# Performance work log

Measured on AMD Instinct MI355X. Metric: run time of the kernel, lower is better.

## Reference

```python
import jax, jax.numpy as jnp
import numpy as np

B, N = 32, 1024


def _pose(points, rot, trans):
    # points: [B,N,3], rot: [B,3,3], trans: [B,3]
    # torch.bmm(points, rot.transpose(1,2)) + trans.unsqueeze(1)
    return jnp.einsum('bni,bji->bnj', points, rot) + trans[:, None, :]


def _l2_dis(pred, target):
    # [B,N] pointwise L2 distance
    return jnp.linalg.norm(pred - target, axis=2)


def _cd_dis(pred, target):
    # symmetric Chamfer-style distance, [B,N]
    p2 = jnp.sum(pred * pred, axis=2)          # [B,N]
    t2 = jnp.sum(target * target, axis=2)      # [B,N]
    cross = jnp.einsum('bnd,bmd->bnm', pred, target)  # [B,N,N]
    d2 = jnp.maximum(p2[:, :, None] + t2[:, None, :] - 2.0 * cross, 0.0)
    dis = jnp.sqrt(d2)                          # [B,N,N]
    dis1 = jnp.min(dis, axis=2)                 # min over target -> [B,N]
    dis2 = jnp.min(dis, axis=1)                 # min over pred   -> [B,N]
    return 0.5 * (dis1 + dis2)


def setup_inputs() -> dict:
    key = jax.random.key(0)
    ks = jax.random.split(key, 8)
    return {
        'delta_rot_pred': jax.random.normal(ks[0], (B, 3, 3), jnp.float32),
        'delta_trans_pred': jax.random.normal(ks[1], (B, 3), jnp.float32),
        'trans_cur': jax.random.normal(ks[2], (B, 3), jnp.float32),
        'rot_cur': jax.random.normal(ks[3], (B, 3, 3), jnp.float32),
        'rot_gt': jax.random.normal(ks[4], (B, 3, 3), jnp.float32),
        'trans_gt': jax.random.normal(ks[5], (B, 3), jnp.float32),
        'points_tmp': jax.random.normal(ks[6], (B, N, 3), jnp.float32),
        'sym_flag': jax.random.uniform(ks[7], (B,), jnp.float32),
    }


def reference(delta_rot_pred, delta_trans_pred, trans_cur, rot_cur, rot_gt, trans_gt, points_tmp, sym_flag):
    posed_pred = _pose(points_tmp, delta_rot_pred, delta_trans_pred)   # [B,N,3]
    posed_gt = _pose(points_tmp, rot_gt, trans_gt)                     # [B,N,3]
    posed_refined = _pose(posed_pred, rot_cur, trans_cur)              # [B,N,3]
    l2 = _l2_dis(posed_refined, posed_gt)                              # [B,N]
    cd = _cd_dis(posed_refined, posed_gt)                              # [B,N]
    per_point = (1.0 - sym_flag)[:, None] * l2 + sym_flag[:, None] * cd
    loss_pose = per_point.mean(axis=1).mean()
    return loss_pose
```

## Files before the change

kernel.cpp:

```cpp
#include <hip/hip_runtime.h>
#include <math.h>

constexpr int B = 32;
constexpr int N = 1024;
constexpr int OCTS = 16;
constexpr int NBLK = B * OCTS;
constexpr int NTHR = 512;
constexpr unsigned short ONE_BF = 0x3F80;

typedef __attribute__((ext_vector_type(8))) short short8;
typedef __attribute__((ext_vector_type(4))) float f32x4;

__device__ __forceinline__ void split_bf(float x, unsigned short& h, unsigned short& l) {
    union { float f; unsigned u; } a; a.f = x;
    unsigned r = (a.u + 0x7FFFu + ((a.u >> 16) & 1u)) >> 16;
    h = (unsigned short)r;
    union { unsigned u; float f; } hb; hb.u = r << 16;
    union { float f; unsigned u; } d; d.f = x - hb.f;
    l = (unsigned short)((d.u + 0x7FFFu + ((d.u >> 16) & 1u)) >> 16);
}
__device__ __forceinline__ unsigned short neg2bf(unsigned short h) {
    return (unsigned short)((h & 0x7FFFu) ? (unsigned short)((h ^ 0x8000u) + 0x0080u)
                                          : (unsigned short)0);
}
__device__ __forceinline__ unsigned pk(unsigned short a, unsigned short b) {
    return (unsigned)a | ((unsigned)b << 16);
}

__global__ __launch_bounds__(NTHR, 4) void chamfer_mfma(
    const float* __restrict__ dR,
    const float* __restrict__ dt,
    const float* __restrict__ tc,
    const float* __restrict__ Rc,
    const float* __restrict__ G,
    const float* __restrict__ g,
    const float* __restrict__ pts,
    const float* __restrict__ sym,
    float* __restrict__ partial)
{
    __shared__ __align__(16) unsigned short Bp[N][16];
    __shared__ __align__(16) unsigned short Bg[N][16];
    __shared__ __align__(16) unsigned short Ap[64][32];
    __shared__ __align__(16) unsigned short Ag[64][32];
    __shared__ float wsum[8];

    const int blk = blockIdx.x;
    const int b   = blk >> 4;
    const int oct = blk & 15;
    const int t   = threadIdx.x;

    const float* dRb = dR + b * 9;
    const float* Rcb = Rc + b * 9;
    const float* Gb  = G  + b * 9;
    const float* dtb = dt + b * 3;
    const float* tcb = tc + b * 3;
    const float* gb  = g  + b * 3;
    const float symb = sym[b];

    float M[9], v[3];
    #pragma unroll
    for (int j = 0; j < 3; ++j) {
        #pragma unroll
        for (int i = 0; i < 3; ++i)
            M[j*3+i] = Rcb[j*3+0]*dRb[0*3+i] + Rcb[j*3+1]*dRb[1*3+i] + Rcb[j*3+2]*dRb[2*3+i];
        v[j] = Rcb[j*3+0]*dtb[0] + Rcb[j*3+1]*dtb[1] + Rcb[j*3+2]*dtb[2] + tcb[j];
    }

    float acc = 0.f;

    {
        const float2* P2 = (const float2*)(pts + (size_t)b * N * 3);
        const float2 u0 = P2[3*t + 0];
        const float2 u1 = P2[3*t + 1];
        const float2 u2 = P2[3*t + 2];
        const float pxs[2] = {u0.x, u1.y};
        const float pys[2] = {u0.y, u2.x};
        const float pzs[2] = {u1.x, u2.y};
        #pragma unroll
        for (int s = 0; s < 2; ++s) {
            const int i = 2*t + s;
            const float px = pxs[s], py = pys[s], pz = pzs[s];
            const float ax = fmaf(M[0],px, fmaf(M[1],py, fmaf(M[2],pz, v[0])));
            const float ay = fmaf(M[3],px, fmaf(M[4],py, fmaf(M[5],pz, v[1])));
            const float az = fmaf(M[6],px, fmaf(M[7],py, fmaf(M[8],pz, v[2])));
            const float cx = fmaf(Gb[0],px, fmaf(Gb[1],py, fmaf(Gb[2],pz, gb[0])));
            const float cy = fmaf(Gb[3],px, fmaf(Gb[4],py, fmaf(Gb[5],pz, gb[1])));
            const float cz = fmaf(Gb[6],px, fmaf(Gb[7],py, fmaf(Gb[8],pz, gb[2])));
            const float a2 = ax*ax + ay*ay + az*az;
            const float c2 = cx*cx + cy*cy + cz*cz;

            if (oct == 0) {
                const float dx = ax - cx, dy = ay - cy, dz = az - cz;
                acc += (1.f - symb) * sqrtf(dx*dx + dy*dy + dz*dz);
            }

            unsigned short axh,axl, ayh,ayl, azh,azl, anh,anl;
            unsigned short cxh,cxl, cyh,cyl, czh,czl, cnh,cnl;
            split_bf(ax,axh,axl); split_bf(ay,ayh,ayl); split_bf(az,azh,azl); split_bf(a2,anh,anl);
            split_bf(cx,cxh,cxl); split_bf(cy,cyh,cyl); split_bf(cz,czh,czl); split_bf(c2,cnh,cnl);

            uint4 bp0 = {pk(axh,ayh), pk(azh,axh), pk(ayh,azh), pk(axl,ayl)};
            uint4 bp1 = {pk(azl,axl), pk(ayl,azl), pk(ONE_BF,ONE_BF), pk(anh,anl)};
            *(uint4*)&Bp[i][0] = bp0; *(uint4*)&Bp[i][8] = bp1;
            uint4 bg0 = {pk(cxh,cyh), pk(czh,cxh), pk(cyh,czh), pk(cxl,cyl)};
            uint4 bg1 = {pk(czl,cxl), pk(cyl,czl), pk(ONE_BF,ONE_BF), pk(cnh,cnl)};
            *(uint4*)&Bg[i][0] = bg0; *(uint4*)&Bg[i][8] = bg1;

            if ((i >> 6) == oct) {
                const int lr = i & 63;
                const unsigned short nxh=neg2bf(axh), nyh=neg2bf(ayh), nzh=neg2bf(azh);
                const unsigned short nxl=neg2bf(axl), nyl=neg2bf(ayl), nzl=neg2bf(azl);
                uint4 a0 = {pk(nxh,nyh), pk(nzh,nxl), pk(nyl,nzl), pk(nxh,nyh)};
                uint4 a1 = {pk(nzh,nxl), pk(nyl,nzl), pk(anh,anl), pk(ONE_BF,ONE_BF)};
                uint4 zz = {0,0,0,0};
                *(uint4*)&Ap[lr][0] = a0; *(uint4*)&Ap[lr][8]  = a1;
                *(uint4*)&Ap[lr][16] = zz; *(uint4*)&Ap[lr][24] = zz;
                const unsigned short mxh=neg2bf(cxh), myh=neg2bf(cyh), mzh=neg2bf(czh);
                const unsigned short mxl=neg2bf(cxl), myl=neg2bf(cyl), mzl=neg2bf(czl);
                uint4 c0 = {pk(mxh,myh), pk(mzh,mxl), pk(myl,mzl), pk(mxh,myh)};
                uint4 c1 = {pk(mzh,mxl), pk(myl,mzl), pk(cnh,cnl), pk(ONE_BF,ONE_BF)};
                *(uint4*)&Ag[lr][0] = c0; *(uint4*)&Ag[lr][8]  = c1;
                *(uint4*)&Ag[lr][16] = zz; *(uint4*)&Ag[lr][24] = zz;
            }
        }
    }
    __syncthreads();

    const int w    = t >> 6;
    const int lane = t & 63;
    const int side = w >> 2;
    const int strip= w & 3;
    const int col  = lane & 15;
    const int kg   = lane >> 4;

    const unsigned short* Abase = (side ? &Ag[0][0] : &Ap[0][0])
                                  + (strip*16 + col) * 32 + kg * 8;
    const unsigned short* Bbase = (side ? &Bp[0][0] : &Bg[0][0])
                                  + col * 16 + (kg & 1) * 8;

    const short8 av = *(const short8*)Abase;
    const f32x4 zero = {0.f, 0.f, 0.f, 0.f};
    float r0 = 3.4e38f, r1 = 3.4e38f, r2 = 3.4e38f, r3 = 3.4e38f;

    #pragma unroll 8
    for (int tile = 0; tile < 64; ++tile) {
        const short8 bv = *(const short8*)(Bbase + tile * 256);
        const f32x4 c = __builtin_amdgcn_mfma_f32_16x16x32_bf16(av, bv, zero, 0, 0, 0);
        r0 = fminf(r0, c[0]); r1 = fminf(r1, c[1]);
        r2 = fminf(r2, c[2]); r3 = fminf(r3, c[3]);
    }

    #pragma unroll
    for (int m = 1; m <= 8; m <<= 1) {
        r0 = fminf(r0, __shfl_xor(r0, m));
        r1 = fminf(r1, __shfl_xor(r1, m));
        r2 = fminf(r2, __shfl_xor(r2, m));
        r3 = fminf(r3, __shfl_xor(r3, m));
    }
    if (col == 0) {
        acc += 0.5f * symb * (sqrtf(fmaxf(r0, 0.f)) + sqrtf(fmaxf(r1, 0.f)) +
                              sqrtf(fmaxf(r2, 0.f)) + sqrtf(fmaxf(r3, 0.f)));
    }

    #pragma unroll
    for (int m = 1; m <= 32; m <<= 1) acc += __shfl_xor(acc, m);
    if (lane == 0) wsum[w] = acc;
    __syncthreads();
    if (t == 0) {
        float s = 0.f;
        #pragma unroll
        for (int j = 0; j < 8; ++j) s += wsum[j];
        partial[blk] = s;
    }
}

__global__ __launch_bounds__(128) void chamfer_final(
    const float* __restrict__ partial, float* __restrict__ out)
{
    __shared__ float wsum[2];
    const int t = threadIdx.x;
    const float4 v = ((const float4*)partial)[t];
    float a = (v.x + v.y) + (v.z + v.w);
    #pragma unroll
    for (int m = 1; m <= 32; m <<= 1) a += __shfl_xor(a, m);
    if ((t & 63) == 0) wsum[t >> 6] = a;
    __syncthreads();
    if (t == 0) out[0] = (wsum[0] + wsum[1]) * (1.0f / (float)(B * N));
}

extern "C" void kernel_launch(void* const* d_in, const int* in_sizes, int n_in,
                              void* d_out, int out_size, void* d_ws, size_t ws_size,
                              hipStream_t stream) {
    const float* dR  = (const float*)d_in[0];
    const float* dt  = (const float*)d_in[1];
    const float* tc  = (const float*)d_in[2];
    const float* Rc  = (const float*)d_in[3];
    const float* G   = (const float*)d_in[4];
    const float* g   = (const float*)d_in[5];
    const float* pts = (const float*)d_in[6];
    const float* sym = (const float*)d_in[7];

    float* partial = (float*)d_ws;
    float* out     = (float*)d_out;

    chamfer_mfma<<<NBLK, NTHR, 0, stream>>>(dR, dt, tc, Rc, G, g, pts, sym, partial);
    chamfer_final<<<1, 128, 0, stream>>>(partial, out);
}
```

Baseline: 15.18 us.

## Switch chamfer min-distance to 32x32x16 MFMA with half as many blocks

Replaces the 16x16x32 bf16 MFMA (which zero-padded half of K) with 32x32x16 MFMA that exactly fits the K=16 split-bf16 encoding. Each wave now covers 32 rows, so each block handles 128 query points and the grid halves to 256 blocks. The B operand is re-laid out in shared memory per 32-column tile. The final reduction kernel shrinks to one wave. Fewer blocks means the per-block pose/pack prologue runs less often, but a 256-block grid may underfill the GPU.

```diff
diff --git a/kernel.cpp b/kernel.cpp
--- a/kernel.cpp
+++ b/kernel.cpp
@@ -3,13 +3,13 @@
 
 constexpr int B = 32;
 constexpr int N = 1024;
-constexpr int OCTS = 16;
+constexpr int OCTS = 8;
 constexpr int NBLK = B * OCTS;
 constexpr int NTHR = 512;
 constexpr unsigned short ONE_BF = 0x3F80;
 
 typedef __attribute__((ext_vector_type(8))) short short8;
-typedef __attribute__((ext_vector_type(4))) float f32x4;
+typedef __attribute__((ext_vector_type(16))) float f32x16;
 
 __device__ __forceinline__ void split_bf(float x, unsigned short& h, unsigned short& l) {
     union { float f; unsigned u; } a; a.f = x;
@@ -38,15 +38,15 @@
     const float* __restrict__ sym,
     float* __restrict__ partial)
 {
-    __shared__ __align__(16) unsigned short Bp[N][16];
-    __shared__ __align__(16) unsigned short Bg[N][16];
-    __shared__ __align__(16) unsigned short Ap[64][32];
-    __shared__ __align__(16) unsigned short Ag[64][32];
+    __shared__ __align__(16) unsigned short BpT[32][2][32][8];
+    __shared__ __align__(16) unsigned short BgT[32][2][32][8];
+    __shared__ __align__(16) unsigned short Ap[128][16];
+    __shared__ __align__(16) unsigned short Ag[128][16];
     __shared__ float wsum[8];
 
     const int blk = blockIdx.x;
-    const int b   = blk >> 4;
-    const int oct = blk & 15;
+    const int b   = blk >> 3;
+    const int oct = blk & 7;
     const int t   = threadIdx.x;
 
     const float* dRb = dR + b * 9;
@@ -99,28 +99,28 @@
             split_bf(ax,axh,axl); split_bf(ay,ayh,ayl); split_bf(az,azh,azl); split_bf(a2,anh,anl);
             split_bf(cx,cxh,cxl); split_bf(cy,cyh,cyl); split_bf(cz,czh,czl); split_bf(c2,cnh,cnl);
 
+            const int tile = i >> 5, c = i & 31;
             uint4 bp0 = {pk(axh,ayh), pk(azh,axh), pk(ayh,azh), pk(axl,ayl)};
             uint4 bp1 = {pk(azl,axl), pk(ayl,azl), pk(ONE_BF,ONE_BF), pk(anh,anl)};
-            *(uint4*)&Bp[i][0] = bp0; *(uint4*)&Bp[i][8] = bp1;
+            *(uint4*)&BpT[tile][0][c][0] = bp0;
+            *(uint4*)&BpT[tile][1][c][0] = bp1;
             uint4 bg0 = {pk(cxh,cyh), pk(czh,cxh), pk(cyh,czh), pk(cxl,cyl)};
             uint4 bg1 = {pk(czl,cxl), pk(cyl,czl), pk(ONE_BF,ONE_BF), pk(cnh,cnl)};
-            *(uint4*)&Bg[i][0] = bg0; *(uint4*)&Bg[i][8] = bg1;
-
-            if ((i >> 6) == oct) {
-                const int lr = i & 63;
+            *(uint4*)&BgT[tile][0][c][0] = bg0;
+            *(uint4*)&BgT[tile][1][c][0] = bg1;
+
+            if ((i >> 7) == oct) {
+                const int lr = i & 127;
                 const unsigned short nxh=neg2bf(axh), nyh=neg2bf(ayh), nzh=neg2bf(azh);
                 const unsigned short nxl=neg2bf(axl), nyl=neg2bf(ayl), nzl=neg2bf(azl);
                 uint4 a0 = {pk(nxh,nyh), pk(nzh,nxl), pk(nyl,nzl), pk(nxh,nyh)};
                 uint4 a1 = {pk(nzh,nxl), pk(nyl,nzl), pk(anh,anl), pk(ONE_BF,ONE_BF)};
-                uint4 zz = {0,0,0,0};
-                *(uint4*)&Ap[lr][0] = a0; *(uint4*)&Ap[lr][8]  = a1;
-                *(uint4*)&Ap[lr][16] = zz; *(uint4*)&Ap[lr][24] = zz;
+                *(uint4*)&Ap[lr][0] = a0; *(uint4*)&Ap[lr][8] = a1;
                 const unsigned short mxh=neg2bf(cxh), myh=neg2bf(cyh), mzh=neg2bf(czh);
                 const unsigned short mxl=neg2bf(cxl), myl=neg2bf(cyl), mzl=neg2bf(czl);
                 uint4 c0 = {pk(mxh,myh), pk(mzh,mxl), pk(myl,mzl), pk(mxh,myh)};
                 uint4 c1 = {pk(mzh,mxl), pk(myl,mzl), pk(cnh,cnl), pk(ONE_BF,ONE_BF)};
-                *(uint4*)&Ag[lr][0] = c0; *(uint4*)&Ag[lr][8]  = c1;
-                *(uint4*)&Ag[lr][16] = zz; *(uint4*)&Ag[lr][24] = zz;
+                *(uint4*)&Ag[lr][0] = c0; *(uint4*)&Ag[lr][8] = c1;
             }
         }
     }
@@ -130,36 +130,40 @@
     const int lane = t & 63;
     const int side = w >> 2;
     const int strip= w & 3;
-    const int col  = lane & 15;
-    const int kg   = lane >> 4;
-
-    const unsigned short* Abase = (side ? &Ag[0][0] : &Ap[0][0])
-                                  + (strip*16 + col) * 32 + kg * 8;
-    const unsigned short* Bbase = (side ? &Bp[0][0] : &Bg[0][0])
-                                  + col * 16 + (kg & 1) * 8;
-
-    const short8 av = *(const short8*)Abase;
-    const f32x4 zero = {0.f, 0.f, 0.f, 0.f};
-    float r0 = 3.4e38f, r1 = 3.4e38f, r2 = 3.4e38f, r3 = 3.4e38f;
+    const int c32  = lane & 31;
+    const int kg   = lane >> 5;
+
+    const unsigned short* Aside = side ? &Ag[0][0] : &Ap[0][0];
+    const short8 av = *(const short8*)(Aside + (strip*32 + c32) * 16 + kg * 8);
+
+    const short8* Bside = (const short8*)(side ? &BpT[0][0][0][0] : &BgT[0][0][0][0]);
+    const short8* Bl = Bside + lane;
+
+    f32x16 mins;
+    #pragma unroll
+    for (int i = 0; i < 16; ++i) mins[i] = 3.4e38f;
 
     #pragma unroll 8
-    for (int tile = 0; tile < 64; ++tile) {
-        const short8 bv = *(const short8*)(Bbase + tile * 256);
-        const f32x4 c = __builtin_amdgcn_mfma_f32_16x16x32_bf16(av, bv, zero, 0, 0, 0);
-        r0 = fminf(r0, c[0]); r1 = fminf(r1, c[1]);
-        r2 = fminf(r2, c[2]); r3 = fminf(r3, c[3]);
-    }
-
-    #pragma unroll
-    for (int m = 1; m <= 8; m <<= 1) {
-        r0 = fminf(r0, __shfl_xor(r0, m));
-        r1 = fminf(r1, __shfl_xor(r1, m));
-        r2 = fminf(r2, __shfl_xor(r2, m));
-        r3 = fminf(r3, __shfl_xor(r3, m));
-    }
-    if (col == 0) {
-        acc += 0.5f * symb * (sqrtf(fmaxf(r0, 0.f)) + sqrtf(fmaxf(r1, 0.f)) +
-                              sqrtf(fmaxf(r2, 0.f)) + sqrtf(fmaxf(r3, 0.f)));
+    for (int tile = 0; tile < 32; ++tile) {
+        const short8 bv = Bl[tile * 64];
+        const f32x16 c = __builtin_amdgcn_mfma_f32_32x32x16_bf16(av, bv, mins*0.f, 0, 0, 0);
+        #pragma unroll
+        for (int i = 0; i < 16; ++i) mins[i] = fminf(mins[i], c[i]);
+    }
+
+    #pragma unroll
+    for (int i = 0; i < 16; ++i) {
+        float m = mins[i];
+        #pragma unroll
+        for (int mm = 1; mm <= 16; mm <<= 1)
+            m = fminf(m, __shfl_xor(m, mm));
+        mins[i] = m;
+    }
+    if (c32 == 0) {
+        float s = 0.f;
+        #pragma unroll
+        for (int i = 0; i < 16; ++i) s += sqrtf(fmaxf(mins[i], 0.f));
+        acc += 0.5f * symb * s;
     }
 
     #pragma unroll
@@ -174,18 +178,15 @@
     }
 }
 
-__global__ __launch_bounds__(128) void chamfer_final(
+__global__ __launch_bounds__(64) void chamfer_final(
     const float* __restrict__ partial, float* __restrict__ out)
 {
-    __shared__ float wsum[2];
     const int t = threadIdx.x;
     const float4 v = ((const float4*)partial)[t];
     float a = (v.x + v.y) + (v.z + v.w);
     #pragma unroll
     for (int m = 1; m <= 32; m <<= 1) a += __shfl_xor(a, m);
-    if ((t & 63) == 0) wsum[t >> 6] = a;
-    __syncthreads();
-    if (t == 0) out[0] = (wsum[0] + wsum[1]) * (1.0f / (float)(B * N));
+    if (t == 0) out[0] = a * (1.0f / (float)(B * N));
 }
 
 extern "C" void kernel_launch(void* const* d_in, const int* in_sizes, int n_in,
@@ -204,5 +205,5 @@
     float* out     = (float*)d_out;
 
     chamfer_mfma<<<NBLK, NTHR, 0, stream>>>(dR, dt, tc, Rc, G, g, pts, sym, partial);
-    chamfer_final<<<1, 128, 0, stream>>>(partial, out);
-}
+    chamfer_final<<<1, 64, 0, stream>>>(partial, out);
+}
```

Measured after the change: 18.81 us. +23.9%, slower.
